# Kernel tuning notes

Hardware: AMD Instinct MI355X
Metric: run time of the kernel (lower is better)

## Reference

```python
import jax, jax.numpy as jnp
import numpy as np

D = 128          # lattice edge (Z = Y = X = 128)
S = 8            # state_size
H = 16           # hidden_size
IN = 7 * S       # own state + 6 neighbor states = 56


def setup_inputs() -> dict:
    key = jax.random.key(0)
    k0, k1, k2 = jax.random.split(key, 3)
    N = D * D * D
    states = jax.random.normal(k0, (N, S), dtype=jnp.float32)
    W1 = jax.random.normal(k1, (IN, H), dtype=jnp.float32) * (1.0 / np.sqrt(IN))
    b1 = jnp.zeros((H,), dtype=jnp.float32)
    W2 = jax.random.normal(k2, (H, S), dtype=jnp.float32) * (1.0 / np.sqrt(H))
    b2 = jnp.zeros((S,), dtype=jnp.float32)
    return {"states": states, "W1": W1, "b1": b1, "W2": W2, "b2": b2}


def reference(states, W1, b1, W2, b2):
    # linear index = z*(X*Y) + y*X + x  ->  grid layout (Z, Y, X, S)
    g = states.reshape(D, D, D, S)
    # 6-neighbor gather with periodic boundary (NEIGHBOR_DIRECTIONS order:
    # (-1,0,0),(1,0,0),(0,-1,0),(0,1,0),(0,0,-1),(0,0,1)); x->axis2, y->axis1, z->axis0.
    # roll(+1) along an axis fetches the neighbor in the -1 direction.
    nbrs = [
        jnp.roll(g,  1, axis=2),  # x-1
        jnp.roll(g, -1, axis=2),  # x+1
        jnp.roll(g,  1, axis=1),  # y-1
        jnp.roll(g, -1, axis=1),  # y+1
        jnp.roll(g,  1, axis=0),  # z-1
        jnp.roll(g, -1, axis=0),  # z+1
    ]
    inp = jnp.concatenate([g] + nbrs, axis=-1)          # (Z, Y, X, 56)
    h = jnp.tanh(jnp.einsum('zyxi,ih->zyxh', inp, W1) + b1)
    out = jnp.einsum('zyxh,hs->zyxs', h, W2) + b2        # (Z, Y, X, 8)
    return out.reshape(-1, S)
```

## Files before the change

kernel.cpp:

```cpp
#include <hip/hip_runtime.h>

#define DIM 128

typedef __attribute__((ext_vector_type(8))) short bf16x8;
typedef __attribute__((ext_vector_type(4))) float f32x4;
typedef __attribute__((ext_vector_type(4))) unsigned int u32x4;

static __device__ __forceinline__ unsigned short f2bf_rne(float f) {
    union { float f; unsigned int i; } c; c.f = f;
    unsigned int u = c.i;
    return (unsigned short)((u + 0x7fffu + ((u >> 16) & 1u)) >> 16);
}
static __device__ __forceinline__ float bf2f(unsigned short u) {
    union { unsigned int i; float f; } c; c.i = ((unsigned int)u) << 16;
    return c.f;
}
static __device__ __forceinline__ unsigned int fbits(float f) {
    union { float f; unsigned int i; } c; c.f = f; return c.i;
}
static __device__ __forceinline__ unsigned int pack_bf16_rne(float lo, float hi) {
    unsigned int ul = fbits(lo), uh = fbits(hi);
    unsigned int tl = ul + 0x7fffu + ((ul >> 16) & 1u);
    unsigned int th = uh + 0x7fffu + ((uh >> 16) & 1u);
    return __builtin_amdgcn_perm(th, tl, 0x07060302u);
}

struct Frags {
    bf16x8 w1h0, w1l0, w1h1, w1l1, w2h, w2l;
    f32x4 b1v, b2v;
};

static __device__ __forceinline__ void build_frags(
    const float* W1, const float* b1, const float* W2, const float* b2,
    int col, int quad, Frags& F)
{
#pragma unroll
    for (int j = 0; j < 8; ++j) {
        int k0 = quad * 8 + j;
        float w = W1[k0 * 16 + col];
        unsigned short hi = f2bf_rne(w);
        F.w1h0[j] = (short)hi;
        F.w1l0[j] = (short)f2bf_rne(w - bf2f(hi));

        int k1 = 32 + quad * 8 + j;
        float wv = (k1 < 56) ? W1[k1 * 16 + col] : 0.0f;
        hi = f2bf_rne(wv);
        F.w1h1[j] = (short)hi;
        F.w1l1[j] = (short)f2bf_rne(wv - bf2f(hi));

        float w2 = (j < 4 && col < 8) ? W2[(quad * 4 + j) * 8 + col] : 0.0f;
        hi = f2bf_rne(w2);
        F.w2h[j] = (short)hi;
        F.w2l[j] = (short)f2bf_rne(w2 - bf2f(hi));
    }
#pragma unroll
    for (int r = 0; r < 4; ++r) {
        F.b1v[r] = b1[quad * 4 + r];
        F.b2v[r] = (quad < 2) ? b2[quad * 4 + r] : 0.0f;
    }
}

__global__ __launch_bounds__(64) void setup_kernel(
    const float* __restrict__ W1, const float* __restrict__ b1,
    const float* __restrict__ W2, const float* __restrict__ b2,
    u32x4* __restrict__ ws)
{
    const int lane = threadIdx.x;
    Frags F;
    build_frags(W1, b1, W2, b2, lane & 15, lane >> 4, F);
    union { bf16x8 v; u32x4 u; } c;
    c.v = F.w1h0; ws[0 * 64 + lane] = c.u;
    c.v = F.w1l0; ws[1 * 64 + lane] = c.u;
    c.v = F.w1h1; ws[2 * 64 + lane] = c.u;
    c.v = F.w1l1; ws[3 * 64 + lane] = c.u;
    c.v = F.w2h;  ws[4 * 64 + lane] = c.u;
    c.v = F.w2l;  ws[5 * 64 + lane] = c.u;
    union { f32x4 v; u32x4 u; } b;
    b.v = F.b1v; ws[6 * 64 + lane] = b.u;
    b.v = F.b2v; ws[7 * 64 + lane] = b.u;
}

template<bool USE_WS>
__global__ __launch_bounds__(256, 2) void lattice_kernel(
    const float* __restrict__ states,
    const float* __restrict__ W1, const float* __restrict__ b1,
    const float* __restrict__ W2, const float* __restrict__ b2,
    float* __restrict__ out, const u32x4* __restrict__ ws)
{
    __shared__ __align__(16) float rows[14 * 1024];

    const int tid  = threadIdx.x;
    const int lane = tid & 63;
    const int wave = tid >> 6;
    const int col  = lane & 15;
    const int quad = lane >> 4;

    Frags F;
    if (USE_WS) {
        union { u32x4 u; bf16x8 v; } c;
        c.u = ws[0 * 64 + lane]; F.w1h0 = c.v;
        c.u = ws[1 * 64 + lane]; F.w1l0 = c.v;
        c.u = ws[2 * 64 + lane]; F.w1h1 = c.v;
        c.u = ws[3 * 64 + lane]; F.w1l1 = c.v;
        c.u = ws[4 * 64 + lane]; F.w2h  = c.v;
        c.u = ws[5 * 64 + lane]; F.w2l  = c.v;
        union { u32x4 u; f32x4 v; } b;
        b.u = ws[6 * 64 + lane]; F.b1v = b.v;
        b.u = ws[7 * 64 + lane]; F.b2v = b.v;
    } else {
        build_frags(W1, b1, W2, b2, col, quad, F);
    }

    const int bI   = blockIdx.x;
    const int slab = bI & 7;
    const int inr  = bI >> 3;
    const int z    = slab * 16 + (inr >> 5);
    const int y0   = (inr & 31) << 2;

    f32x4 tmp[14];
#pragma unroll
    for (int i = 0; i < 14; ++i) {
        const int c  = wave * 14 + i;
        const int r  = c >> 2;
        const int p  = c & 3;
        int yr, zr;
        if (r < 6)       { yr = (y0 - 1 + r) & 127; zr = z; }
        else if (r < 10) { yr = y0 + (r - 6);       zr = (z - 1) & 127; }
        else             { yr = y0 + (r - 10);      zr = (z + 1) & 127; }
        const float* g = states + (size_t)(zr * 16384 + yr * 128) * 8 + p * 256 + (lane << 2);
        tmp[i] = *(const f32x4*)g;
    }
#pragma unroll
    for (int i = 0; i < 14; ++i) {
        const int c = wave * 14 + i;
        const int r = c >> 2;
        const int p = c & 3;
        *(f32x4*)(&rows[r * 1024 + p * 256 + (lane << 2)]) = tmp[i];
    }
    __syncthreads();

    const int rA  = (quad == 3) ? wave : wave + 1;
    const int dxA = (quad == 1) ? -1 : (quad == 2) ? 1 : 0;
    const int rB  = (quad == 1) ? 6 + wave : (quad == 2) ? 10 + wave : wave + 2;

    const int outrow = z * 16384 + (y0 + wave) * 128;

#pragma unroll
    for (int i = 0; i < 8; ++i) {
        const int X  = i << 4;
        const int xA = (X + col + dxA) & 127;
        const float* pA = &rows[rA * 1024 + xA * 8];
        f32x4 a0 = *(const f32x4*)pA;
        f32x4 a1 = *(const f32x4*)(pA + 4);
        const float* pB = &rows[rB * 1024 + (X + col) * 8];
        f32x4 c0 = *(const f32x4*)pB;
        f32x4 c1 = *(const f32x4*)(pB + 4);

        union { bf16x8 v; unsigned int u[4]; } s0f, s1f;
        s0f.u[0] = __builtin_amdgcn_perm(fbits(a0[1]), fbits(a0[0]), 0x07060302u);
        s0f.u[1] = __builtin_amdgcn_perm(fbits(a0[3]), fbits(a0[2]), 0x07060302u);
        s0f.u[2] = __builtin_amdgcn_perm(fbits(a1[1]), fbits(a1[0]), 0x07060302u);
        s0f.u[3] = __builtin_amdgcn_perm(fbits(a1[3]), fbits(a1[2]), 0x07060302u);
        s1f.u[0] = __builtin_amdgcn_perm(fbits(c0[1]), fbits(c0[0]), 0x07060302u);
        s1f.u[1] = __builtin_amdgcn_perm(fbits(c0[3]), fbits(c0[2]), 0x07060302u);
        s1f.u[2] = __builtin_amdgcn_perm(fbits(c1[1]), fbits(c1[0]), 0x07060302u);
        s1f.u[3] = __builtin_amdgcn_perm(fbits(c1[3]), fbits(c1[2]), 0x07060302u);

        f32x4 acc = F.b1v;
        acc = __builtin_amdgcn_mfma_f32_16x16x32_bf16(F.w1h0, s0f.v, acc, 0, 0, 0);
        acc = __builtin_amdgcn_mfma_f32_16x16x32_bf16(F.w1l0, s0f.v, acc, 0, 0, 0);
        acc = __builtin_amdgcn_mfma_f32_16x16x32_bf16(F.w1h1, s1f.v, acc, 0, 0, 0);
        acc = __builtin_amdgcn_mfma_f32_16x16x32_bf16(F.w1l1, s1f.v, acc, 0, 0, 0);

        float h0t, h1t, h2t, h3t;
        {
            float e;
            e = __expf(2.0f * acc[0]); h0t = 1.0f - 2.0f * __builtin_amdgcn_rcpf(e + 1.0f);
            e = __expf(2.0f * acc[1]); h1t = 1.0f - 2.0f * __builtin_amdgcn_rcpf(e + 1.0f);
            e = __expf(2.0f * acc[2]); h2t = 1.0f - 2.0f * __builtin_amdgcn_rcpf(e + 1.0f);
            e = __expf(2.0f * acc[3]); h3t = 1.0f - 2.0f * __builtin_amdgcn_rcpf(e + 1.0f);
        }
        union { bf16x8 v; unsigned int u[4]; } hf;
        hf.u[0] = pack_bf16_rne(h0t, h1t);
        hf.u[1] = pack_bf16_rne(h2t, h3t);
        hf.u[2] = 0u;
        hf.u[3] = 0u;

        f32x4 acc2 = F.b2v;
        acc2 = __builtin_amdgcn_mfma_f32_16x16x32_bf16(F.w2h, hf.v, acc2, 0, 0, 0);
        acc2 = __builtin_amdgcn_mfma_f32_16x16x32_bf16(F.w2l, hf.v, acc2, 0, 0, 0);

        if (quad < 2) {
            *(f32x4*)(out + (size_t)(outrow + X + col) * 8 + quad * 4) = acc2;
        }
    }
}

extern "C" void kernel_launch(void* const* d_in, const int* in_sizes, int n_in,
                              void* d_out, int out_size, void* d_ws, size_t ws_size,
                              hipStream_t stream) {
    const float* states = (const float*)d_in[0];
    const float* W1     = (const float*)d_in[1];
    const float* b1     = (const float*)d_in[2];
    const float* W2     = (const float*)d_in[3];
    const float* b2     = (const float*)d_in[4];
    float* out          = (float*)d_out;

    const bool use_ws = ws_size >= (size_t)(8 * 64 * 16);
    if (use_ws) {
        hipLaunchKernelGGL(setup_kernel, dim3(1), dim3(64), 0, stream,
                           W1, b1, W2, b2, (u32x4*)d_ws);
        hipLaunchKernelGGL((lattice_kernel<true>), dim3(4096), dim3(256), 0, stream,
                           states, W1, b1, W2, b2, out, (const u32x4*)d_ws);
    } else {
        hipLaunchKernelGGL((lattice_kernel<false>), dim3(4096), dim3(256), 0, stream,
                           states, W1, b1, W2, b2, out, (const u32x4*)d_ws);
    }
}
```

Baseline: 133.6 us.

## Store staged lattice rows in LDS as bf16 with padded slots

Input rows are converted from fp32 to bf16 once, during staging into shared memory, rather than on every MFMA operand load. This halves the LDS footprint per block, which lets launch bounds request four blocks per CU instead of two. Slot strides are padded, with a spare slot between the z-1 and z+1 row groups, to spread accesses across LDS banks. Output stores become nontemporal. The trade-offs are more register pressure under the tighter occupancy bound, plus a different global-load pattern in which each lane fetches a full 8-float state with two 16-byte loads.

```diff
diff --git a/kernel.cpp b/kernel.cpp
--- a/kernel.cpp
+++ b/kernel.cpp
@@ -80,14 +80,15 @@
     b.v = F.b2v; ws[7 * 64 + lane] = b.u;
 }
 
+#define SLOT_STRIDE 2064
 template<bool USE_WS>
-__global__ __launch_bounds__(256, 2) void lattice_kernel(
+__global__ __launch_bounds__(256, 4) void lattice_kernel(
     const float* __restrict__ states,
     const float* __restrict__ W1, const float* __restrict__ b1,
     const float* __restrict__ W2, const float* __restrict__ b2,
     float* __restrict__ out, const u32x4* __restrict__ ws)
 {
-    __shared__ __align__(16) float rows[14 * 1024];
+    __shared__ __align__(16) unsigned char lds[15 * SLOT_STRIDE];
 
     const int tid  = threadIdx.x;
     const int lane = tid & 63;
@@ -117,31 +118,39 @@
     const int z    = slab * 16 + (inr >> 5);
     const int y0   = (inr & 31) << 2;
 
-    f32x4 tmp[14];
-#pragma unroll
-    for (int i = 0; i < 14; ++i) {
-        const int c  = wave * 14 + i;
-        const int r  = c >> 2;
-        const int p  = c & 3;
+    f32x4 ga[7], gb[7];
+    int   laddr[7];
+#pragma unroll
+    for (int i = 0; i < 7; ++i) {
+        const int tk   = wave * 7 + i;
+        const int slot = (tk < 20) ? (tk >> 1) : 11 + ((tk - 20) >> 1);
+        const int half = tk & 1;
         int yr, zr;
-        if (r < 6)       { yr = (y0 - 1 + r) & 127; zr = z; }
-        else if (r < 10) { yr = y0 + (r - 6);       zr = (z - 1) & 127; }
-        else             { yr = y0 + (r - 10);      zr = (z + 1) & 127; }
-        const float* g = states + (size_t)(zr * 16384 + yr * 128) * 8 + p * 256 + (lane << 2);
-        tmp[i] = *(const f32x4*)g;
-    }
-#pragma unroll
-    for (int i = 0; i < 14; ++i) {
-        const int c = wave * 14 + i;
-        const int r = c >> 2;
-        const int p = c & 3;
-        *(f32x4*)(&rows[r * 1024 + p * 256 + (lane << 2)]) = tmp[i];
+        if (slot < 6)       { yr = (y0 - 1 + slot) & 127; zr = z; }
+        else if (slot < 10) { yr = y0 + (slot - 6);       zr = (z - 1) & 127; }
+        else                { yr = y0 + (slot - 11);      zr = (z + 1) & 127; }
+        const int c = half * 64 + lane;
+        const float* g = states + ((size_t)(zr * 16384 + yr * 128 + c) << 3);
+        ga[i] = *(const f32x4*)g;
+        gb[i] = *(const f32x4*)(g + 4);
+        laddr[i] = slot * SLOT_STRIDE + c * 16;
+    }
+#pragma unroll
+    for (int i = 0; i < 7; ++i) {
+        u32x4 p;
+        p[0] = __builtin_amdgcn_perm(fbits(ga[i][1]), fbits(ga[i][0]), 0x07060302u);
+        p[1] = __builtin_amdgcn_perm(fbits(ga[i][3]), fbits(ga[i][2]), 0x07060302u);
+        p[2] = __builtin_amdgcn_perm(fbits(gb[i][1]), fbits(gb[i][0]), 0x07060302u);
+        p[3] = __builtin_amdgcn_perm(fbits(gb[i][3]), fbits(gb[i][2]), 0x07060302u);
+        *(u32x4*)(lds + laddr[i]) = p;
     }
     __syncthreads();
 
-    const int rA  = (quad == 3) ? wave : wave + 1;
-    const int dxA = (quad == 1) ? -1 : (quad == 2) ? 1 : 0;
-    const int rB  = (quad == 1) ? 6 + wave : (quad == 2) ? 10 + wave : wave + 2;
+    const int dxA   = (quad == 1) ? -1 : (quad == 2) ? 1 : 0;
+    const int slotA = (quad == 3) ? wave : wave + 1;
+    const int slotB = (quad == 1) ? 6 + wave : (quad == 2) ? 11 + wave : wave + 2;
+    const int baseA = slotA * SLOT_STRIDE;
+    const int baseB = slotB * SLOT_STRIDE;
 
     const int outrow = z * 16384 + (y0 + wave) * 128;
 
@@ -149,28 +158,14 @@
     for (int i = 0; i < 8; ++i) {
         const int X  = i << 4;
         const int xA = (X + col + dxA) & 127;
-        const float* pA = &rows[rA * 1024 + xA * 8];
-        f32x4 a0 = *(const f32x4*)pA;
-        f32x4 a1 = *(const f32x4*)(pA + 4);
-        const float* pB = &rows[rB * 1024 + (X + col) * 8];
-        f32x4 c0 = *(const f32x4*)pB;
-        f32x4 c1 = *(const f32x4*)(pB + 4);
-
-        union { bf16x8 v; unsigned int u[4]; } s0f, s1f;
-        s0f.u[0] = __builtin_amdgcn_perm(fbits(a0[1]), fbits(a0[0]), 0x07060302u);
-        s0f.u[1] = __builtin_amdgcn_perm(fbits(a0[3]), fbits(a0[2]), 0x07060302u);
-        s0f.u[2] = __builtin_amdgcn_perm(fbits(a1[1]), fbits(a1[0]), 0x07060302u);
-        s0f.u[3] = __builtin_amdgcn_perm(fbits(a1[3]), fbits(a1[2]), 0x07060302u);
-        s1f.u[0] = __builtin_amdgcn_perm(fbits(c0[1]), fbits(c0[0]), 0x07060302u);
-        s1f.u[1] = __builtin_amdgcn_perm(fbits(c0[3]), fbits(c0[2]), 0x07060302u);
-        s1f.u[2] = __builtin_amdgcn_perm(fbits(c1[1]), fbits(c1[0]), 0x07060302u);
-        s1f.u[3] = __builtin_amdgcn_perm(fbits(c1[3]), fbits(c1[2]), 0x07060302u);
+        bf16x8 s0f = *(const bf16x8*)(lds + baseA + xA * 16);
+        bf16x8 s1f = *(const bf16x8*)(lds + baseB + (X + col) * 16);
 
         f32x4 acc = F.b1v;
-        acc = __builtin_amdgcn_mfma_f32_16x16x32_bf16(F.w1h0, s0f.v, acc, 0, 0, 0);
-        acc = __builtin_amdgcn_mfma_f32_16x16x32_bf16(F.w1l0, s0f.v, acc, 0, 0, 0);
-        acc = __builtin_amdgcn_mfma_f32_16x16x32_bf16(F.w1h1, s1f.v, acc, 0, 0, 0);
-        acc = __builtin_amdgcn_mfma_f32_16x16x32_bf16(F.w1l1, s1f.v, acc, 0, 0, 0);
+        acc = __builtin_amdgcn_mfma_f32_16x16x32_bf16(F.w1h0, s0f, acc, 0, 0, 0);
+        acc = __builtin_amdgcn_mfma_f32_16x16x32_bf16(F.w1l0, s0f, acc, 0, 0, 0);
+        acc = __builtin_amdgcn_mfma_f32_16x16x32_bf16(F.w1h1, s1f, acc, 0, 0, 0);
+        acc = __builtin_amdgcn_mfma_f32_16x16x32_bf16(F.w1l1, s1f, acc, 0, 0, 0);
 
         float h0t, h1t, h2t, h3t;
         {
@@ -191,7 +186,8 @@
         acc2 = __builtin_amdgcn_mfma_f32_16x16x32_bf16(F.w2l, hf.v, acc2, 0, 0, 0);
 
         if (quad < 2) {
-            *(f32x4*)(out + (size_t)(outrow + X + col) * 8 + quad * 4) = acc2;
+            f32x4* p = (f32x4*)(out + (size_t)(outrow + X + col) * 8 + quad * 4);
+            __builtin_nontemporal_store(acc2, p);
         }
     }
 }
```

Measured after the change: 135.3 us. Within noise of the previous version (+1.2%).
